# Kernel optimization log

Measured on AMD Instinct MI355X. Metric: run time of the kernel, lower is better.

The kernel has to match this reference:

```python
import jax, jax.numpy as jnp
import numpy as np

N = 10000      # number of keypoints / graph nodes
CIN = 512      # in_channels
COUT = 512     # out_channels
KCHEB = 5      # Chebyshev order K
KNN = 20       # k nearest neighbors


def setup_inputs() -> dict:
    key = jax.random.key(0)
    k1, k2, k3, k4 = jax.random.split(key, 4)
    x = jax.random.normal(k1, (1, CIN, N), dtype=jnp.float32)
    position = jax.random.normal(k2, (1, N, 3), dtype=jnp.float32)
    # ChebConv weights: one [CIN, COUT] matrix per Chebyshev order, plus bias
    theta = jax.random.normal(k3, (KCHEB, CIN, COUT), dtype=jnp.float32) / np.float32(np.sqrt(CIN * KCHEB))
    bias = jax.random.normal(k4, (COUT,), dtype=jnp.float32) * 0.01
    return {"x": x, "position": position, "theta": theta, "bias": bias, "knn": KNN}


def reference(x, position, theta, bias, knn):
    # ---- knn_graph(position.squeeze(0), k, flow='target_to_source') ----
    pos = position[0]                       # [N, 3]
    n = pos.shape[0]
    sq = jnp.sum(pos * pos, axis=1)
    d2 = sq[:, None] + sq[None, :] - 2.0 * (pos @ pos.T)   # [N, N] squared dists
    d2 = jnp.where(jnp.eye(n, dtype=bool), jnp.inf, d2)    # exclude self (loop=False)
    _, nbr = jax.lax.top_k(-d2, knn)        # [N, knn] nearest neighbor indices
    # flow='target_to_source' => edge_index = [center, neighbor]
    row = jnp.repeat(jnp.arange(n), knn)    # edge source (center) for ChebConv
    col = nbr.reshape(-1)                   # edge target (neighbor)

    # ---- ChebConv sym normalization, lambda_max=2 => L_hat = -D^-1/2 A D^-1/2 ----
    deg = jnp.zeros((n,), x.dtype).at[row].add(jnp.float32(1.0))
    dis = jnp.where(deg > 0, jax.lax.rsqrt(deg), jnp.float32(0.0))
    w = -dis[row] * dis[col]                # [E] edge weights, zero diagonal

    h = jnp.swapaxes(x, 1, 2)               # [B, N, CIN]

    def prop(t):
        # out[target] += w * t[source]  (sparse L_hat @ t)
        msg = t[:, row, :] * w[None, :, None]
        return jnp.zeros_like(t).at[:, col, :].add(msg)

    # Chebyshev recurrence: Tx0 = h, Tx1 = L_hat h, Tx_k = 2 L_hat Tx_{k-1} - Tx_{k-2}
    Tx0 = h
    out = jnp.einsum('bnc,co->bno', Tx0, theta[0])
    Tx1 = prop(Tx0)
    out = out + jnp.einsum('bnc,co->bno', Tx1, theta[1])
    for k in range(2, theta.shape[0]):
        Tx2 = 2.0 * prop(Tx1) - Tx0
        out = out + jnp.einsum('bnc,co->bno', Tx2, theta[k])
        Tx0, Tx1 = Tx1, Tx2
    out = out + bias
    return jnp.swapaxes(out, 1, 2)          # [B, COUT, N]
```

## Files before the change

kernel.cpp:

```cpp
#include <hip/hip_runtime.h>
#include <hip/hip_bf16.h>
#include <cstdint>
#include <cstddef>

#define N_NODES 10000
#define KNN_K 20
#define NEDGE (N_NODES * KNN_K)
#define NBATCH 157
#define POS4_PAD 10048
#define NCELL 4096
#define NPX 1250
#define GM_PAIRS 628

using bf16x8 = __attribute__((ext_vector_type(8))) short;
using f32x4  = __attribute__((ext_vector_type(4))) float;

__device__ __forceinline__ float bf_lo(unsigned int u) {
  union { unsigned int i; float f; } c; c.i = u << 16; return c.f;
}
__device__ __forceinline__ float bf_hi(unsigned int u) {
  union { unsigned int i; float f; } c; c.i = u & 0xFFFF0000u; return c.f;
}
__device__ __forceinline__ unsigned short f2bf(float f) {
  union { float f; unsigned int i; } c; c.f = f;
  unsigned int u = c.i;
  u += 0x7FFFu + ((u >> 16) & 1u);
  return (unsigned short)(u >> 16);
}

__device__ __forceinline__ void gll16(const void* g, void* l) {
  __builtin_amdgcn_global_load_lds(
      (const __attribute__((address_space(1))) unsigned int*)g,
      (__attribute__((address_space(3))) unsigned int*)l,
      16, 0, 0);
}

__global__ __launch_bounds__(256) void transpose_f32_bf16(
    const float* __restrict__ src0, unsigned short* __restrict__ dst,
    int srows, int scols, int dstride, size_t slice_elems, int dcol_per_slice)
{
  __shared__ float lds[64 * 65];
  const int z = blockIdx.z;
  const float* src = src0 + (size_t)z * slice_elems;
  const int dcol0 = z * dcol_per_slice;
  const int c0 = blockIdx.x * 64;
  const int r0 = blockIdx.y * 64;
  const int tid = threadIdx.x;
#pragma unroll
  for (int q = 0; q < 4; ++q) {
    int unit = q * 256 + tid;
    int rr = unit >> 4;
    int cu = unit & 15;
    int r = r0 + rr, c = c0 + cu * 4;
    float4 v = make_float4(0.f, 0.f, 0.f, 0.f);
    if (r < srows && c + 3 < scols) v = *(const float4*)&src[(size_t)r * scols + c];
    lds[rr * 65 + cu * 4 + 0] = v.x;
    lds[rr * 65 + cu * 4 + 1] = v.y;
    lds[rr * 65 + cu * 4 + 2] = v.z;
    lds[rr * 65 + cu * 4 + 3] = v.w;
  }
  __syncthreads();
#pragma unroll
  for (int q = 0; q < 2; ++q) {
    int unit = q * 256 + tid;
    int cl = unit >> 3;
    int ru = unit & 7;
    int c = c0 + cl;
    if (c < scols) {
      unsigned short tmp[8];
#pragma unroll
      for (int j = 0; j < 8; ++j) tmp[j] = f2bf(lds[(ru * 8 + j) * 65 + cl]);
      uint4 o;
      o.x = (unsigned int)tmp[0] | ((unsigned int)tmp[1] << 16);
      o.y = (unsigned int)tmp[2] | ((unsigned int)tmp[3] << 16);
      o.z = (unsigned int)tmp[4] | ((unsigned int)tmp[5] << 16);
      o.w = (unsigned int)tmp[6] | ((unsigned int)tmp[7] << 16);
      *(uint4*)&dst[(size_t)c * dstride + dcol0 + r0 + ru * 8] = o;
    }
  }
}

__global__ __launch_bounds__(256) void pos4_kernel(
    const float* __restrict__ pos, float4* __restrict__ pos4,
    int* __restrict__ counts, int* __restrict__ cursor,
    int* __restrict__ cellid, int* __restrict__ cellcnt,
    int* __restrict__ nfail)
{
  int c = blockIdx.x * 256 + threadIdx.x;
  if (c == 0) *nfail = 0;
  if (c < POS4_PAD) {
    float4 v;
    if (c < N_NODES) {
      float x = pos[c * 3 + 0], y = pos[c * 3 + 1], z = pos[c * 3 + 2];
      v = make_float4(x, y, z, x * x + y * y + z * z);
      int cx = min(15, max(0, (int)floorf((x + 4.0f) * 2.0f)));
      int cy = min(15, max(0, (int)floorf((y + 4.0f) * 2.0f)));
      int cz = min(15, max(0, (int)floorf((z + 4.0f) * 2.0f)));
      int cell = (cx << 8) | (cy << 4) | cz;
      cellid[c] = cell;
      atomicAdd(&cellcnt[cell], 1);
      counts[c] = 0; cursor[c] = 0;
    } else {
      v = make_float4(0.f, 0.f, 0.f, __builtin_inff());
    }
    pos4[c] = v;
  }
}

__global__ __launch_bounds__(256) void cellscan_kernel(
    const int* __restrict__ cellcnt, int* __restrict__ cellptr)
{
  __shared__ int part[256];
  const int tid = threadIdx.x;
  const int base = tid * 16;
  int cv[16];
  int s = 0;
#pragma unroll
  for (int q = 0; q < 4; ++q) {
    int4 v = *(const int4*)&cellcnt[base + q * 4];
    cv[q * 4 + 0] = v.x; cv[q * 4 + 1] = v.y;
    cv[q * 4 + 2] = v.z; cv[q * 4 + 3] = v.w;
    s += v.x + v.y + v.z + v.w;
  }
  part[tid] = s;
  __syncthreads();
  for (int off = 1; off < 256; off <<= 1) {
    int add = (tid >= off) ? part[tid - off] : 0;
    __syncthreads();
    part[tid] += add;
    __syncthreads();
  }
  int run = part[tid] - s;
#pragma unroll
  for (int q = 0; q < 16; ++q) { cellptr[base + q] = run; run += cv[q]; }
  if (tid == 255) cellptr[NCELL] = run;
}

__global__ __launch_bounds__(256) void perm_kernel(
    const int* __restrict__ cellid, const int* __restrict__ cellptr,
    int* __restrict__ cellcur, int* __restrict__ perm,
    const float4* __restrict__ pos4, float4* __restrict__ pos4s)
{
  int c = blockIdx.x * 256 + threadIdx.x;
  if (c < N_NODES) {
    int cell = cellid[c];
    int p = atomicAdd(&cellcur[cell], 1);
    int slot = cellptr[cell] + p;
    perm[slot] = c;
    pos4s[slot] = pos4[c];
  }
}

__device__ __forceinline__ float knn_dist(float4 pi, float4 s) {
  float dot = fmaf(pi.x, s.x, fmaf(pi.y, s.y, pi.z * s.z));
  return fmaf(-2.0f, dot, pi.w + s.w);
}

__device__ __forceinline__ void insert8(float r[8], float k) {
  asm("v_med3_f32 %0, %1, %2, %3" : "=v"(r[7]) : "v"(k), "v"(r[6]), "v"(r[7]));
  asm("v_med3_f32 %0, %1, %2, %3" : "=v"(r[6]) : "v"(k), "v"(r[5]), "v"(r[6]));
  asm("v_med3_f32 %0, %1, %2, %3" : "=v"(r[5]) : "v"(k), "v"(r[4]), "v"(r[5]));
  asm("v_med3_f32 %0, %1, %2, %3" : "=v"(r[4]) : "v"(k), "v"(r[3]), "v"(r[4]));
  asm("v_med3_f32 %0, %1, %2, %3" : "=v"(r[3]) : "v"(k), "v"(r[2]), "v"(r[3]));
  asm("v_med3_f32 %0, %1, %2, %3" : "=v"(r[2]) : "v"(k), "v"(r[1]), "v"(r[2]));
  asm("v_med3_f32 %0, %1, %2, %3" : "=v"(r[1]) : "v"(k), "v"(r[0]), "v"(r[1]));
  r[0] = fminf(r[0], k);
}

__device__ __forceinline__ float merge_tau20(float r[8], int lane) {
  const float INF = __builtin_inff();
  float tau = INF;
#pragma unroll
  for (int t = 0; t < KNN_K; ++t) {
    float m = r[0];
    m = fminf(m, __shfl_xor(m, 1));
    m = fminf(m, __shfl_xor(m, 2));
    m = fminf(m, __shfl_xor(m, 4));
    m = fminf(m, __shfl_xor(m, 8));
    m = fminf(m, __shfl_xor(m, 16));
    m = fminf(m, __shfl_xor(m, 32));
    unsigned long long who = __ballot(r[0] == m);
    int srcl = __ffsll(who) - 1;
    if (lane == srcl) {
#pragma unroll
      for (int z = 0; z < 7; ++z) r[z] = r[z + 1];
      r[7] = INF;
    }
    tau = m;
  }
  return tau;
}

__device__ __forceinline__ void emit_hits(
    int i, bool valid, float d, float tau, int cid, int lane, int& cnt,
    int* __restrict__ knn_out)
{
  unsigned long long less = __ballot(valid && d < tau);
  unsigned long long eq   = __ballot(valid && d == tau);
  if (less) {
    if (valid && d < tau) {
      int pos = cnt + (int)__popcll(less & ((1ull << lane) - 1ull));
      if (pos < KNN_K) knn_out[i * KNN_K + pos] = cid;
    }
    cnt += (int)__popcll(less);
  }
  if (eq && cnt < KNN_K) {
    if (valid && d == tau) {
      int pos = cnt + (int)__popcll(eq & ((1ull << lane) - 1ull));
      if (pos < KNN_K) knn_out[i * KNN_K + pos] = cid;
    }
    cnt = min(KNN_K, cnt + (int)__popcll(eq));
  }
}

__global__ __launch_bounds__(256) void knn_try_kernel(
    const float4* __restrict__ pos4, const float4* __restrict__ pos4s,
    const int* __restrict__ perm, const int* __restrict__ cellptr,
    int* __restrict__ knn_out, int* __restrict__ wl, int* __restrict__ nfail)
{
  const int lane = threadIdx.x & 63, wave = threadIdx.x >> 6;
  const int wid = blockIdx.x * 4 + wave;
  const int i = perm[wid];
  const float4 pi = pos4[i];
  const float INF = __builtin_inff();

  const int cx = min(15, max(0, (int)floorf((pi.x + 4.0f) * 2.0f)));
  const int cy = min(15, max(0, (int)floorf((pi.y + 4.0f) * 2.0f)));
  const int cz = min(15, max(0, (int)floorf((pi.z + 4.0f) * 2.0f)));
  const int x0 = max(cx - 1, 0), x1 = min(cx + 1, 15);
  const int y0 = max(cy - 1, 0), y1 = min(cy + 1, 15);
  const int z0 = max(cz - 1, 0), z1 = min(cz + 1, 15);

  float r[8];
#pragma unroll
  for (int q = 0; q < 8; ++q) r[q] = INF;

  for (int X = x0; X <= x1; ++X)
    for (int Y = y0; Y <= y1; ++Y) {
      const int cb = (X << 8) | (Y << 4);
      const int s0 = cellptr[cb + z0], s1 = cellptr[cb + z1 + 1];
      for (int c0 = s0; c0 < s1; c0 += 64) {
        const int slot = c0 + lane;
        const int idx = min(slot, s1 - 1);
        const float4 s = pos4s[idx];
        const int nid = perm[idx];
        float d = knn_dist(pi, s);
        float k = (slot < s1 && nid != i) ? d : INF;
        insert8(r, k);
      }
    }
  float tau = merge_tau20(r, lane);

  float mx = INF, my = INF, mz = INF;
  if (x0 > 0)  mx = pi.x - (x0 * 0.5f - 4.0f);
  if (x1 < 15) mx = fminf(mx, ((x1 + 1) * 0.5f - 4.0f) - pi.x);
  if (y0 > 0)  my = pi.y - (y0 * 0.5f - 4.0f);
  if (y1 < 15) my = fminf(my, ((y1 + 1) * 0.5f - 4.0f) - pi.y);
  if (z0 > 0)  mz = pi.z - (z0 * 0.5f - 4.0f);
  if (z1 < 15) mz = fminf(mz, ((z1 + 1) * 0.5f - 4.0f) - pi.z);
  const float marg = fminf(mx, fminf(my, mz));

  if (tau < marg * marg) {
    int cnt = 0;
    for (int X = x0; X <= x1; ++X)
      for (int Y = y0; Y <= y1; ++Y) {
        const int cb = (X << 8) | (Y << 4);
        const int s0 = cellptr[cb + z0], s1 = cellptr[cb + z1 + 1];
        for (int c0 = s0; c0 < s1; c0 += 64) {
          const int slot = c0 + lane;
          const int idx = min(slot, s1 - 1);
          const float4 s = pos4s[idx];
          const int nid = perm[idx];
          float d = knn_dist(pi, s);
          bool valid = (slot < s1) && (nid != i);
          emit_hits(i, valid, d, tau, nid, lane, cnt, knn_out);
        }
      }
    return;
  }

  if (lane == 0) {
    int slot = atomicAdd(nfail, 1);
    wl[slot] = i;
  }
}

__global__ __launch_bounds__(256) void knn_full_kernel(
    const float4* __restrict__ pos4, const int* __restrict__ wl,
    const int* __restrict__ nfail, int* __restrict__ knn_out)
{
  __shared__ float wmin[4];
  __shared__ int lcnt, eqcnt;
  __shared__ int eqbuf[64];
  const int tid = threadIdx.x;
  const int lane = tid & 63, wave = tid >> 6;
  const float INF = __builtin_inff();
  const int nf = *nfail;

  for (int w = blockIdx.x; w < nf; w += 2500) {
    const int i = wl[w];
    const float4 pi = pos4[i];

    float r[8];
#pragma unroll
    for (int q = 0; q < 8; ++q) r[q] = INF;
    for (int b = wave; b < NBATCH; b += 4) {
      const int cid = b * 64 + lane;
      const float4 s = pos4[cid];
      float d = knn_dist(pi, s);
      float k = (cid == i) ? INF : d;
      insert8(r, k);
    }

    float tau = INF;
#pragma unroll
    for (int t = 0; t < KNN_K; ++t) {
      float m = r[0];
      m = fminf(m, __shfl_xor(m, 1));
      m = fminf(m, __shfl_xor(m, 2));
      m = fminf(m, __shfl_xor(m, 4));
      m = fminf(m, __shfl_xor(m, 8));
      m = fminf(m, __shfl_xor(m, 16));
      m = fminf(m, __shfl_xor(m, 32));
      if (lane == 0) wmin[wave] = m;
      __syncthreads();
      float m0 = wmin[0], m1 = wmin[1], m2 = wmin[2], m3 = wmin[3];
      float gm = fminf(fminf(m0, m1), fminf(m2, m3));
      int wsel = (m0 == gm) ? 0 : ((m1 == gm) ? 1 : ((m2 == gm) ? 2 : 3));
      __syncthreads();
      if (wave == wsel) {
        unsigned long long who = __ballot(r[0] == gm);
        int srcl = __ffsll(who) - 1;
        if (lane == srcl) {
#pragma unroll
          for (int z = 0; z < 7; ++z) r[z] = r[z + 1];
          r[7] = INF;
        }
      }
      tau = gm;
    }

    if (tid == 0) { lcnt = 0; eqcnt = 0; }
    __syncthreads();
    for (int b = wave; b < NBATCH; b += 4) {
      const int cid = b * 64 + lane;
      const float4 s = pos4[cid];
      float d = knn_dist(pi, s);
      bool valid = (cid != i);
      if (valid && d < tau) {
        int slot = atomicAdd(&lcnt, 1);
        if (slot < KNN_K) knn_out[i * KNN_K + slot] = cid;
      }
      if (valid && d == tau) {
        int e = atomicAdd(&eqcnt, 1);
        if (e < 64) eqbuf[e] = cid;
      }
    }
    __syncthreads();
    if (tid == 0) {
      int base = lcnt;
      int ne = min(eqcnt, 64);
      for (int a = 1; a < ne; ++a) {
        int v = eqbuf[a];
        int b2 = a - 1;
        while (b2 >= 0 && eqbuf[b2] > v) { eqbuf[b2 + 1] = eqbuf[b2]; --b2; }
        eqbuf[b2 + 1] = v;
      }
      for (int q = 0; q < ne && base + q < KNN_K; ++q)
        knn_out[i * KNN_K + base + q] = eqbuf[q];
    }
    __syncthreads();
  }
}

__global__ __launch_bounds__(256) void count_kernel(
    const int* __restrict__ knn, int* __restrict__ counts)
{
  int e = blockIdx.x * 256 + threadIdx.x;
  if (e < NEDGE) atomicAdd(&counts[knn[e]], 1);
}

__global__ __launch_bounds__(256) void scan_kernel(
    const int* __restrict__ counts, int* __restrict__ rptr)
{
  __shared__ int part[256];
  const int tid = threadIdx.x;
  const int base = tid * 40;
  int s = 0;
  int cv[40];
  if (tid < 250) {
#pragma unroll
    for (int q = 0; q < 10; ++q) {
      int4 v = *(const int4*)&counts[base + q * 4];
      cv[q * 4 + 0] = v.x; cv[q * 4 + 1] = v.y;
      cv[q * 4 + 2] = v.z; cv[q * 4 + 3] = v.w;
      s += v.x + v.y + v.z + v.w;
    }
  }
  part[tid] = s;
  __syncthreads();
  for (int off = 1; off < 256; off <<= 1) {
    int add = (tid >= off) ? part[tid - off] : 0;
    __syncthreads();
    part[tid] += add;
    __syncthreads();
  }
  int run = part[tid] - s;
  if (tid < 250) {
#pragma unroll
    for (int q = 0; q < 40; ++q) { rptr[base + q] = run; run += cv[q]; }
  }
  if (tid == 255) rptr[N_NODES] = run;
}

__global__ __launch_bounds__(256) void fill_kernel(
    const int* __restrict__ knn, const int* __restrict__ rptr,
    int* __restrict__ cursor, int* __restrict__ rsrc)
{
  int e = blockIdx.x * 256 + threadIdx.x;
  if (e < NEDGE) {
    int j = knn[e];
    int i = e / KNN_K;
    int p = atomicAdd(&cursor[j], 1);
    rsrc[rptr[j] + p] = i;
  }
}

__global__ __launch_bounds__(256) void sort_kernel(
    const int* __restrict__ rptr, int* __restrict__ rsrc)
{
  const int lane = threadIdx.x & 63, wave = threadIdx.x >> 6;
  const int j = blockIdx.x * 4 + wave;
  const int s0 = rptr[j], s1 = rptr[j + 1], deg = s1 - s0;
  if (deg <= 64) {
    int v = (lane < deg) ? rsrc[s0 + lane] : 0x7FFFFFFF;
#pragma unroll
    for (int k = 2; k <= 64; k <<= 1) {
#pragma unroll
      for (int m = k >> 1; m > 0; m >>= 1) {
        int other = __shfl_xor(v, m);
        bool up = ((lane & k) == 0);
        bool lower = ((lane & m) == 0);
        v = (up == lower) ? min(v, other) : max(v, other);
      }
    }
    if (lane < deg) rsrc[s0 + lane] = v;
  } else if (lane == 0) {
    for (int a = s0 + 1; a < s1; ++a) {
      int v = rsrc[a];
      int b = a - 1;
      while (b >= s0 && rsrc[b] > v) { rsrc[b + 1] = rsrc[b]; --b; }
      rsrc[b + 1] = v;
    }
  }
}

__global__ __launch_bounds__(256) void prop_kernel(
    const unsigned short* __restrict__ tin, const unsigned short* __restrict__ tprev,
    unsigned short* __restrict__ tout, const int* __restrict__ rptr,
    const int* __restrict__ rsrc, const int* __restrict__ perm, float scale2)
{
  const int wave = threadIdx.x >> 6, lane = threadIdx.x & 63;
  const int b = blockIdx.x;
  const int xcd = b & 7, qb = b >> 3;
  const int local = qb * 4 + wave;
  if (local >= NPX) return;
  const int j = perm[xcd * NPX + local];
  const int s0 = rptr[j], s1 = rptr[j + 1];
  const size_t coff = (size_t)lane * 8;

  float a0[8], a1[8], a2[8], a3[8];
#pragma unroll
  for (int q = 0; q < 8; ++q) { a0[q] = 0.f; a1[q] = 0.f; a2[q] = 0.f; a3[q] = 0.f; }

  for (int base = s0; base < s1; base += 64) {
    const int clen = min(64, s1 - base);
    int myidx = (base + lane < s1) ? rsrc[base + lane] : 0;
    int t = 0;
    for (; t + 4 <= clen; t += 4) {
      int i0 = __shfl(myidx, t);
      int i1 = __shfl(myidx, t + 1);
      int i2 = __shfl(myidx, t + 2);
      int i3 = __shfl(myidx, t + 3);
      uint4 v0 = *(const uint4*)&tin[(size_t)i0 * 512 + coff];
      uint4 v1 = *(const uint4*)&tin[(size_t)i1 * 512 + coff];
      uint4 v2 = *(const uint4*)&tin[(size_t)i2 * 512 + coff];
      uint4 v3 = *(const uint4*)&tin[(size_t)i3 * 512 + coff];
      a0[0] += bf_lo(v0.x); a0[1] += bf_hi(v0.x); a0[2] += bf_lo(v0.y); a0[3] += bf_hi(v0.y);
      a0[4] += bf_lo(v0.z); a0[5] += bf_hi(v0.z); a0[6] += bf_lo(v0.w); a0[7] += bf_hi(v0.w);
      a1[0] += bf_lo(v1.x); a1[1] += bf_hi(v1.x); a1[2] += bf_lo(v1.y); a1[3] += bf_hi(v1.y);
      a1[4] += bf_lo(v1.z); a1[5] += bf_hi(v1.z); a1[6] += bf_lo(v1.w); a1[7] += bf_hi(v1.w);
      a2[0] += bf_lo(v2.x); a2[1] += bf_hi(v2.x); a2[2] += bf_lo(v2.y); a2[3] += bf_hi(v2.y);
      a2[4] += bf_lo(v2.z); a2[5] += bf_hi(v2.z); a2[6] += bf_lo(v2.w); a2[7] += bf_hi(v2.w);
      a3[0] += bf_lo(v3.x); a3[1] += bf_hi(v3.x); a3[2] += bf_lo(v3.y); a3[3] += bf_hi(v3.y);
      a3[4] += bf_lo(v3.z); a3[5] += bf_hi(v3.z); a3[6] += bf_lo(v3.w); a3[7] += bf_hi(v3.w);
    }
    for (; t < clen; ++t) {
      int i0 = __shfl(myidx, t);
      uint4 v0 = *(const uint4*)&tin[(size_t)i0 * 512 + coff];
      a0[0] += bf_lo(v0.x); a0[1] += bf_hi(v0.x); a0[2] += bf_lo(v0.y); a0[3] += bf_hi(v0.y);
      a0[4] += bf_lo(v0.z); a0[5] += bf_hi(v0.z); a0[6] += bf_lo(v0.w); a0[7] += bf_hi(v0.w);
    }
  }

  float pv[8] = {0.f, 0.f, 0.f, 0.f, 0.f, 0.f, 0.f, 0.f};
  if (tprev != nullptr) {
    uint4 p = *(const uint4*)&tprev[(size_t)j * 512 + coff];
    pv[0] = bf_lo(p.x); pv[1] = bf_hi(p.x);
    pv[2] = bf_lo(p.y); pv[3] = bf_hi(p.y);
    pv[4] = bf_lo(p.z); pv[5] = bf_hi(p.z);
    pv[6] = bf_lo(p.w); pv[7] = bf_hi(p.w);
  }
  unsigned short o16[8];
#pragma unroll
  for (int q = 0; q < 8; ++q) {
    float acc = (a0[q] + a1[q]) + (a2[q] + a3[q]);
    o16[q] = f2bf(scale2 * acc - pv[q]);
  }
  uint4 o;
  o.x = (unsigned int)o16[0] | ((unsigned int)o16[1] << 16);
  o.y = (unsigned int)o16[2] | ((unsigned int)o16[3] << 16);
  o.z = (unsigned int)o16[4] | ((unsigned int)o16[5] << 16);
  o.w = (unsigned int)o16[6] | ((unsigned int)o16[7] << 16);
  *(uint4*)&tout[(size_t)j * 512 + coff] = o;
}

__global__ __launch_bounds__(256) void gemm_kernel(
    const unsigned short* __restrict__ A,
    const unsigned short* __restrict__ Bt,
    const float* __restrict__ bias,
    float* __restrict__ C)
{
  __shared__ __align__(16) char smem[49152];
  float* eps = (float*)smem;

  const int tid = threadIdx.x;
  const int wave = tid >> 6, lane = tid & 63;
  const int l15 = lane & 15, hi = lane >> 4;

  const int bid = blockIdx.x;
  const int xcd = bid & 7, local = bid >> 3;
  const int qd = GM_PAIRS >> 3, rem = GM_PAIRS & 7;
  const int cnt = (xcd < rem) ? qd + 1 : qd;
  if (local >= cnt) return;
  const int start = (xcd < rem) ? xcd * (qd + 1) : rem * (qd + 1) + (xcd - rem) * qd;
  const int pair = start + local;
  const int n0 = (pair >> 2) * 64;
  const int o0 = (pair & 3) * 128;

  f32x4 acc[4][2];
#pragma unroll
  for (int a = 0; a < 4; ++a)
#pragma unroll
    for (int b = 0; b < 2; ++b) acc[a][b] = (f32x4){0.f, 0.f, 0.f, 0.f};

  auto stage = [&](int kt, int sel) {
    const int k0 = kt * 64;
    const int ko = k0 >> 9;
    const int c0 = k0 & 511;
    const unsigned short* Ab = A + (size_t)ko * ((size_t)N_NODES * 512);
    unsigned short* As = (unsigned short*)(smem + sel * 24576);
    unsigned short* Bs = As + 64 * 64;
#pragma unroll
    for (int q = 0; q < 2; ++q) {
      int idx = (wave * 2 + q) * 64 + lane;
      int r = idx >> 3, u = idx & 7;
      int ug = u ^ (r & 7);
      gll16(Ab + (size_t)(n0 + r) * 512 + c0 + ug * 8, As + (size_t)(wave * 2 + q) * 512);
    }
#pragma unroll
    for (int q = 0; q < 4; ++q) {
      int idx = (wave * 4 + q) * 64 + lane;
      int r = idx >> 3, u = idx & 7;
      int ug = u ^ (r & 7);
      gll16(Bt + (size_t)(o0 + r) * 2560 + k0 + ug * 8, Bs + (size_t)(wave * 4 + q) * 512);
    }
  };

  stage(0, 0);
  asm volatile("s_waitcnt vmcnt(0)" ::: "memory");
  __builtin_amdgcn_s_barrier();

  for (int kt = 0; kt < 40; ++kt) {
    const int cur = kt & 1;
    if (kt + 1 < 40) {
      stage(kt + 1, cur ^ 1);
      asm volatile("s_waitcnt vmcnt(6)" ::: "memory");
    } else {
      asm volatile("s_waitcnt vmcnt(0)" ::: "memory");
    }
    __builtin_amdgcn_s_barrier();
    __builtin_amdgcn_sched_barrier(0);
    unsigned short* As = (unsigned short*)(smem + cur * 24576);
    unsigned short* Bs = As + 64 * 64;
#pragma unroll
    for (int kk = 0; kk < 2; ++kk) {
      bf16x8 af[4], bfr[2];
#pragma unroll
      for (int mi = 0; mi < 4; ++mi) {
        int row = mi * 16 + l15;
        int up = (kk * 4 + hi) ^ (row & 7);
        af[mi] = *(const bf16x8*)(As + row * 64 + up * 8);
      }
#pragma unroll
      for (int ni = 0; ni < 2; ++ni) {
        int row = wave * 32 + ni * 16 + l15;
        int up = (kk * 4 + hi) ^ (row & 7);
        bfr[ni] = *(const bf16x8*)(Bs + row * 64 + up * 8);
      }
#pragma unroll
      for (int mi = 0; mi < 4; ++mi)
#pragma unroll
        for (int ni = 0; ni < 2; ++ni)
          acc[mi][ni] = __builtin_amdgcn_mfma_f32_16x16x32_bf16(af[mi], bfr[ni], acc[mi][ni], 0, 0, 0);
    }
    __builtin_amdgcn_s_barrier();
  }

  __syncthreads();
#pragma unroll
  for (int mi = 0; mi < 4; ++mi)
#pragma unroll
    for (int ni = 0; ni < 2; ++ni) {
      int o_l = wave * 32 + ni * 16 + l15;
      int nb = mi * 16 + hi * 4;
      *(f32x4*)&eps[o_l * 68 + nb] = acc[mi][ni];
    }
  __syncthreads();
#pragma unroll
  for (int q = 0; q < 8; ++q) {
    int unit = q * 256 + tid;
    int o_l = unit >> 4, nu = unit & 15;
    int n = n0 + nu * 4;
    if (n < N_NODES) {
      int o = o0 + o_l;
      f32x4 v = *(const f32x4*)&eps[o_l * 68 + nu * 4];
      float bo = bias[o];
      v = v + bo;
      *(f32x4*)&C[(size_t)o * N_NODES + n] = v;
    }
  }
}

extern "C" void kernel_launch(void* const* d_in, const int* in_sizes, int n_in,
                              void* d_out, int out_size, void* d_ws, size_t ws_size,
                              hipStream_t stream)
{
  const float* x        = (const float*)d_in[0];
  const float* position = (const float*)d_in[1];
  const float* theta    = (const float*)d_in[2];
  const float* bias     = (const float*)d_in[3];

  char* ws = (char*)d_ws;
  size_t off = 0;
  auto alloc = [&](size_t bytes) -> void* {
    void* p = ws + off;
    off = (off + bytes + 255) & ~(size_t)255;
    return p;
  };
  unsigned short* TxAll   = (unsigned short*)alloc(5ull * N_NODES * 512 * 2 + 131072);
  unsigned short* thetabT = (unsigned short*)alloc(512ull * 2560 * 2);
  float4* pos4  = (float4*)alloc((size_t)POS4_PAD * 16);
  float4* pos4s = (float4*)alloc((size_t)N_NODES * 16);
  int* knn    = (int*)alloc((size_t)NEDGE * 4);
  int* rptr   = (int*)alloc((size_t)(N_NODES + 1) * 4);
  int* counts = (int*)alloc((size_t)N_NODES * 4);
  int* cursor = (int*)alloc((size_t)N_NODES * 4);
  int* rsrc   = (int*)alloc((size_t)NEDGE * 4);
  int* cellcnt = (int*)alloc((size_t)NCELL * 4);
  int* cellcur = (int*)alloc((size_t)NCELL * 4);
  int* cellptr = (int*)alloc((size_t)(NCELL + 1) * 4);
  int* cellid  = (int*)alloc((size_t)N_NODES * 4);
  int* perm    = (int*)alloc((size_t)N_NODES * 4);
  int* wl      = (int*)alloc((size_t)N_NODES * 4);
  int* nfail   = (int*)alloc(256);
  if (ws_size < off) return;

  transpose_f32_bf16<<<dim3(8, 8, 5), 256, 0, stream>>>(
      theta, thetabT, 512, 512, 2560, (size_t)512 * 512, 512);
  transpose_f32_bf16<<<dim3(157, 8, 1), 256, 0, stream>>>(
      x, TxAll, 512, N_NODES, 512, 0, 0);

  hipMemsetAsync(cellcnt, 0, (size_t)((char*)cellptr - (char*)cellcnt), stream);
  pos4_kernel<<<40, 256, 0, stream>>>(position, pos4, counts, cursor, cellid, cellcnt, nfail);
  cellscan_kernel<<<1, 256, 0, stream>>>(cellcnt, cellptr);
  perm_kernel<<<40, 256, 0, stream>>>(cellid, cellptr, cellcur, perm, pos4, pos4s);

  knn_try_kernel<<<2500, 256, 0, stream>>>(pos4, pos4s, perm, cellptr, knn, wl, nfail);
  knn_full_kernel<<<2500, 256, 0, stream>>>(pos4, wl, nfail, knn);

  count_kernel<<<(NEDGE + 255) / 256, 256, 0, stream>>>(knn, counts);
  scan_kernel<<<1, 256, 0, stream>>>(counts, rptr);
  fill_kernel<<<(NEDGE + 255) / 256, 256, 0, stream>>>(knn, rptr, cursor, rsrc);
  sort_kernel<<<2500, 256, 0, stream>>>(rptr, rsrc);

  unsigned short* Tx0 = TxAll;
  unsigned short* Tx1 = TxAll + 1ull * N_NODES * 512;
  unsigned short* Tx2 = TxAll + 2ull * N_NODES * 512;
  unsigned short* Tx3 = TxAll + 3ull * N_NODES * 512;
  unsigned short* Tx4 = TxAll + 4ull * N_NODES * 512;

  prop_kernel<<<2504, 256, 0, stream>>>(Tx0, nullptr, Tx1, rptr, rsrc, perm, -0.05f);
  prop_kernel<<<2504, 256, 0, stream>>>(Tx1, Tx0,     Tx2, rptr, rsrc, perm, -0.10f);
  prop_kernel<<<2504, 256, 0, stream>>>(Tx2, Tx1,     Tx3, rptr, rsrc, perm, -0.10f);
  prop_kernel<<<2504, 256, 0, stream>>>(Tx3, Tx2,     Tx4, rptr, rsrc, perm, -0.10f);

  gemm_kernel<<<632, 256, 0, stream>>>(TxAll, thetabT, bias, (float*)d_out);
}
```

Before: 224.9 us.

## Load GEMM B fragments directly to registers and fold memset into transpose

The GEMM kernel stops staging the theta (B) tile through LDS and instead has each wave load its B fragments straight from global memory into registers at the start of every k-step. This cuts LDS use and the B-side LDS writes and reads, which may raise occupancy, but the global loads are less coalesced and sit on the critical path without double buffering. The separate hipMemsetAsync that cleared the cell counters is also dropped; the first transpose launch now zeroes that buffer (8 blocks x 256 threads x 4 ints, which covers both cellcnt and cellcur), removing one launch.

```diff
diff --git a/kernel.cpp b/kernel.cpp
--- a/kernel.cpp
+++ b/kernel.cpp
@@ -37,10 +37,15 @@
 
 __global__ __launch_bounds__(256) void transpose_f32_bf16(
     const float* __restrict__ src0, unsigned short* __restrict__ dst,
-    int srows, int scols, int dstride, size_t slice_elems, int dcol_per_slice)
+    int srows, int scols, int dstride, size_t slice_elems, int dcol_per_slice,
+    int* __restrict__ zbuf)
 {
   __shared__ float lds[64 * 65];
   const int z = blockIdx.z;
+  if (zbuf != nullptr && z == 0 && blockIdx.y == 0 && blockIdx.x < 8) {
+    int4 zz = make_int4(0, 0, 0, 0);
+    *(int4*)&zbuf[(blockIdx.x * 256 + threadIdx.x) * 4] = zz;
+  }
   const float* src = src0 + (size_t)z * slice_elems;
   const int dcol0 = z * dcol_per_slice;
   const int c0 = blockIdx.x * 64;
@@ -531,7 +536,7 @@
     const float* __restrict__ bias,
     float* __restrict__ C)
 {
-  __shared__ __align__(16) char smem[49152];
+  __shared__ __align__(16) char smem[35840];
   float* eps = (float*)smem;
 
   const int tid = threadIdx.x;
@@ -554,13 +559,12 @@
 #pragma unroll
     for (int b = 0; b < 2; ++b) acc[a][b] = (f32x4){0.f, 0.f, 0.f, 0.f};
 
-  auto stage = [&](int kt, int sel) {
+  auto stageA = [&](int kt, int sel) {
     const int k0 = kt * 64;
     const int ko = k0 >> 9;
     const int c0 = k0 & 511;
     const unsigned short* Ab = A + (size_t)ko * ((size_t)N_NODES * 512);
-    unsigned short* As = (unsigned short*)(smem + sel * 24576);
-    unsigned short* Bs = As + 64 * 64;
+    unsigned short* As = (unsigned short*)(smem + sel * 8192);
 #pragma unroll
     for (int q = 0; q < 2; ++q) {
       int idx = (wave * 2 + q) * 64 + lane;
@@ -568,34 +572,36 @@
       int ug = u ^ (r & 7);
       gll16(Ab + (size_t)(n0 + r) * 512 + c0 + ug * 8, As + (size_t)(wave * 2 + q) * 512);
     }
-#pragma unroll
-    for (int q = 0; q < 4; ++q) {
-      int idx = (wave * 4 + q) * 64 + lane;
-      int r = idx >> 3, u = idx & 7;
-      int ug = u ^ (r & 7);
-      gll16(Bt + (size_t)(o0 + r) * 2560 + k0 + ug * 8, Bs + (size_t)(wave * 4 + q) * 512);
-    }
   };
 
-  stage(0, 0);
+  stageA(0, 0);
   asm volatile("s_waitcnt vmcnt(0)" ::: "memory");
   __builtin_amdgcn_s_barrier();
 
   for (int kt = 0; kt < 40; ++kt) {
     const int cur = kt & 1;
+    const int k0c = kt * 64;
+    bf16x8 bfr[2][2];
+#pragma unroll
+    for (int kk = 0; kk < 2; ++kk)
+#pragma unroll
+      for (int ni = 0; ni < 2; ++ni) {
+        int o = o0 + wave * 32 + ni * 16 + l15;
+        bfr[kk][ni] = *(const bf16x8*)(Bt + (size_t)o * 2560 + k0c + kk * 32 + hi * 8);
+      }
+    __builtin_amdgcn_sched_barrier(0);
     if (kt + 1 < 40) {
-      stage(kt + 1, cur ^ 1);
-      asm volatile("s_waitcnt vmcnt(6)" ::: "memory");
+      stageA(kt + 1, cur ^ 1);
+      asm volatile("s_waitcnt vmcnt(2)" ::: "memory");
     } else {
       asm volatile("s_waitcnt vmcnt(0)" ::: "memory");
     }
     __builtin_amdgcn_s_barrier();
     __builtin_amdgcn_sched_barrier(0);
-    unsigned short* As = (unsigned short*)(smem + cur * 24576);
-    unsigned short* Bs = As + 64 * 64;
+    unsigned short* As = (unsigned short*)(smem + cur * 8192);
 #pragma unroll
     for (int kk = 0; kk < 2; ++kk) {
-      bf16x8 af[4], bfr[2];
+      bf16x8 af[4];
 #pragma unroll
       for (int mi = 0; mi < 4; ++mi) {
         int row = mi * 16 + l15;
@@ -603,16 +609,10 @@
         af[mi] = *(const bf16x8*)(As + row * 64 + up * 8);
       }
 #pragma unroll
-      for (int ni = 0; ni < 2; ++ni) {
-        int row = wave * 32 + ni * 16 + l15;
-        int up = (kk * 4 + hi) ^ (row & 7);
-        bfr[ni] = *(const bf16x8*)(Bs + row * 64 + up * 8);
-      }
-#pragma unroll
       for (int mi = 0; mi < 4; ++mi)
 #pragma unroll
         for (int ni = 0; ni < 2; ++ni)
-          acc[mi][ni] = __builtin_amdgcn_mfma_f32_16x16x32_bf16(af[mi], bfr[ni], acc[mi][ni], 0, 0, 0);
+          acc[mi][ni] = __builtin_amdgcn_mfma_f32_16x16x32_bf16(af[mi], bfr[kk][ni], acc[mi][ni], 0, 0, 0);
     }
     __builtin_amdgcn_s_barrier();
   }
@@ -677,11 +677,10 @@
   if (ws_size < off) return;
 
   transpose_f32_bf16<<<dim3(8, 8, 5), 256, 0, stream>>>(
-      theta, thetabT, 512, 512, 2560, (size_t)512 * 512, 512);
+      theta, thetabT, 512, 512, 2560, (size_t)512 * 512, 512, cellcnt);
   transpose_f32_bf16<<<dim3(157, 8, 1), 256, 0, stream>>>(
-      x, TxAll, 512, N_NODES, 512, 0, 0);
-
-  hipMemsetAsync(cellcnt, 0, (size_t)((char*)cellptr - (char*)cellcnt), stream);
+      x, TxAll, 512, N_NODES, 512, 0, 0, nullptr);
+
   pos4_kernel<<<40, 256, 0, stream>>>(position, pos4, counts, cursor, cellid, cellcnt, nfail);
   cellscan_kernel<<<1, 256, 0, stream>>>(cellcnt, cellptr);
   perm_kernel<<<40, 256, 0, stream>>>(cellid, cellptr, cellcur, perm, pos4, pos4s);
```

Result: slower. 257.2 us (+14.4%).
